# Optimization experiments

Hardware: AMD Instinct MI355X
Metric: run time of the kernel (lower is better)

The kernel has to match this reference:

```python
import jax, jax.numpy as jnp
import numpy as np

D = 256       # d_model
HEADS = 8     # n_heads
PTS = 4       # n_points
FF = 1024     # dim_feedforward
HD = D // HEADS
B, Q = 8, 900
HH, WW = 100, 100


def setup_inputs() -> dict:
    key = jax.random.key(0)
    ks = iter(jax.random.split(key, 40))
    p = lambda shape: jax.random.normal(next(ks), shape, dtype=jnp.float32) * 0.02
    inp = {
        "tgt": jax.random.normal(next(ks), (B, Q, D), dtype=jnp.float32),
        "memory": jax.random.normal(next(ks), (B, HH * WW, D), dtype=jnp.float32),
        "H": HH,
        "W": WW,
        # self-attention (nn.MultiheadAttention) params
        "in_proj_w": p((3 * D, D)), "in_proj_b": p((3 * D,)),
        "out_proj_w": p((D, D)), "out_proj_b": p((D,)),
        # layer norms
        "norm1_s": jnp.ones((D,)), "norm1_b": jnp.zeros((D,)),
        "norm2_s": jnp.ones((D,)), "norm2_b": jnp.zeros((D,)),
        "norm3_s": jnp.ones((D,)), "norm3_b": jnp.zeros((D,)),
        # deformable cross-attention params
        "vproj_w": p((D, D)), "vproj_b": p((D,)),
        "offs_w": p((HEADS * PTS * 2, D)), "offs_b": p((HEADS * PTS * 2,)),
        "attw_w": p((HEADS * PTS, D)), "attw_b": p((HEADS * PTS,)),
        "ref_w": p((2, D)), "ref_b": p((2,)),
        "cout_w": p((D, D)), "cout_b": p((D,)),
        # FFN params
        "ffn_w1": p((FF, D)), "ffn_b1": p((FF,)),
        "ffn_w2": p((D, FF)), "ffn_b2": p((D,)),
    }
    return inp


def _layer_norm(x, s, b):
    m = jnp.mean(x, -1, keepdims=True)
    v = jnp.mean((x - m) ** 2, -1, keepdims=True)
    return (x - m) * jax.lax.rsqrt(v + 1e-5) * s + b


def _mha(x, wi, bi, wo, bo):
    b, q, _ = x.shape
    qkv = x @ wi.T + bi
    qh, kh, vh = jnp.split(qkv, 3, axis=-1)
    qh = qh.reshape(b, q, HEADS, HD).transpose(0, 2, 1, 3)
    kh = kh.reshape(b, q, HEADS, HD).transpose(0, 2, 1, 3)
    vh = vh.reshape(b, q, HEADS, HD).transpose(0, 2, 1, 3)
    att = jax.nn.softmax(jnp.einsum('bhqd,bhkd->bhqk', qh, kh) / np.float32(np.sqrt(HD)), axis=-1)
    o = jnp.einsum('bhqk,bhkd->bhqd', att, vh).transpose(0, 2, 1, 3).reshape(b, q, D)
    return o @ wo.T + bo


def _deform_attn(q, mem, H, W, vproj_w, vproj_b, offs_w, offs_b, attw_w, attw_b,
                 ref_w, ref_b, cout_w, cout_b):
    b, nq, _ = q.shape
    # per-query normalized reference points (x, y) in [0,1]
    ref = jax.nn.sigmoid(q @ ref_w.T + ref_b)                         # [B,Q,2]
    offs = (q @ offs_w.T + offs_b).reshape(b, nq, HEADS, PTS, 2)      # [B,Q,h,p,2]
    attw = jax.nn.softmax((q @ attw_w.T + attw_b).reshape(b, nq, HEADS, PTS), axis=-1)
    val = (mem @ vproj_w.T + vproj_b).reshape(b, H * W, HEADS, HD).transpose(0, 2, 1, 3)  # [B,h,HW,hd]
    wh = jnp.array([W, H], dtype=q.dtype)
    loc = ref[:, :, None, None, :] + offs / wh                        # normalized sampling loc
    x = loc[..., 0] * W - 0.5                                         # pixel coords (align_corners=False)
    y = loc[..., 1] * H - 0.5
    x0 = jnp.floor(x); y0 = jnp.floor(y)
    lx = x - x0; ly = y - y0
    x0i = x0.astype(jnp.int32); y0i = y0.astype(jnp.int32)

    def gather(xi, yi):
        valid = ((xi >= 0) & (xi < W) & (yi >= 0) & (yi < H)).astype(q.dtype)
        idx = jnp.clip(yi, 0, H - 1) * W + jnp.clip(xi, 0, W - 1)     # [B,Q,h,p]
        idxt = idx.transpose(0, 2, 1, 3).reshape(b, HEADS, nq * PTS, 1)
        g = jnp.take_along_axis(val, idxt, axis=2)                    # [B,h,Q*p,hd]
        g = g.reshape(b, HEADS, nq, PTS, HD).transpose(0, 2, 1, 3, 4)  # [B,Q,h,p,hd]
        return g * valid[..., None]

    samp = (gather(x0i, y0i) * ((1 - lx) * (1 - ly))[..., None]
            + gather(x0i + 1, y0i) * (lx * (1 - ly))[..., None]
            + gather(x0i, y0i + 1) * ((1 - lx) * ly)[..., None]
            + gather(x0i + 1, y0i + 1) * (lx * ly)[..., None])        # [B,Q,h,p,hd]
    out = jnp.sum(samp * attw[..., None], axis=3).reshape(b, nq, D)
    return out @ cout_w.T + cout_b


def reference(tgt, memory, H, W, in_proj_w, in_proj_b, out_proj_w, out_proj_b,
              norm1_s, norm1_b, norm2_s, norm2_b, norm3_s, norm3_b,
              vproj_w, vproj_b, offs_w, offs_b, attw_w, attw_b, ref_w, ref_b,
              cout_w, cout_b, ffn_w1, ffn_b1, ffn_w2, ffn_b2):
    t2 = _mha(tgt, in_proj_w, in_proj_b, out_proj_w, out_proj_b)
    t = _layer_norm(tgt + t2, norm1_s, norm1_b)
    t2 = _deform_attn(t, memory, H, W, vproj_w, vproj_b, offs_w, offs_b,
                      attw_w, attw_b, ref_w, ref_b, cout_w, cout_b)
    t = _layer_norm(t + t2, norm2_s, norm2_b)
    f = jnp.maximum(t @ ffn_w1.T + ffn_b1, 0) @ ffn_w2.T + ffn_b2
    return _layer_norm(t + f, norm3_s, norm3_b)
```

## Files before the change

### kernel.cpp

```cpp
#include <hip/hip_runtime.h>
#include <hip/hip_bf16.h>

typedef __hip_bfloat16 bf16;
typedef __attribute__((ext_vector_type(8))) short short8;
typedef __attribute__((ext_vector_type(4))) float f32x4;

#define BB 8
#define QQ 900
#define DD 256
#define NH 8
#define HD 32
#define NPTS 4
#define FFD 1024
#define HH 100
#define WW2 100
#define HWTOT 10000

#define QT 64
#define KTC 128
#define NCHUNK ((QQ + KTC - 1) / KTC)
#define QB 4
#define VTP 1024

__device__ inline float tofloat(float x) { return x; }
__device__ inline float tofloat(bf16 x) { return __bfloat162float(x); }
__device__ inline float bf2f(unsigned short u) {
    return __uint_as_float(((unsigned int)u) << 16);
}
__device__ inline void storev(bf16* p, float v) { *p = __float2bfloat16(v); }
__device__ inline void storev(float* p, float v) { *p = v; }

__device__ inline void load4(const float* p, float* v) {
    const float4 t = *(const float4*)p;
    v[0] = t.x; v[1] = t.y; v[2] = t.z; v[3] = t.w;
}
__device__ inline void load4(const bf16* p, float* v) {
    const ushort4 t = *(const ushort4*)p;
    v[0] = bf2f(t.x); v[1] = bf2f(t.y); v[2] = bf2f(t.z); v[3] = bf2f(t.w);
}
__device__ inline void store4(float* p, const float* v) {
    float4 t = {v[0], v[1], v[2], v[3]};
    *(float4*)p = t;
}
__device__ inline void store4(bf16* p, const float* v) {
    bf16 t[4] = {__float2bfloat16(v[0]), __float2bfloat16(v[1]),
                 __float2bfloat16(v[2]), __float2bfloat16(v[3])};
    *(uint2*)p = *(const uint2*)t;
}

typedef __attribute__((address_space(1))) const unsigned int gas_u32;
typedef __attribute__((address_space(3))) unsigned int las_u32;
__device__ inline void gload_lds16(const bf16* g, bf16* l) {
    __builtin_amdgcn_global_load_lds(
        (gas_u32*)(unsigned long long)(const void*)g,
        (las_u32*)(unsigned int)(unsigned long long)(const void*)l, 16, 0, 0);
}

__global__ void pack_kernel(const float* __restrict__ in_proj_w, const float* __restrict__ out_proj_w,
                            const float* __restrict__ cout_w, const float* __restrict__ ffn_w1,
                            const float* __restrict__ ffn_w2, const float* __restrict__ vproj_w,
                            const float* __restrict__ offs_w, const float* __restrict__ attw_w,
                            const float* __restrict__ ref_w, const float* __restrict__ offs_b,
                            const float* __restrict__ attw_b, const float* __restrict__ ref_b,
                            const float* __restrict__ tgt, bf16* __restrict__ wpk,
                            bf16* __restrict__ tgtb, float* __restrict__ dbias,
                            bf16* __restrict__ vt) {
    const int idx = blockIdx.x * 256 + threadIdx.x;
    const int TOT = 950272 + 1843200 + 128 + 2097152;
    if (idx >= TOT) return;
    if (idx < 196608) {
        wpk[idx] = __float2bfloat16(in_proj_w[idx]);
    } else if (idx < 262144) {
        wpk[idx] = __float2bfloat16(out_proj_w[idx - 196608]);
    } else if (idx < 327680) {
        wpk[idx] = __float2bfloat16(cout_w[idx - 262144]);
    } else if (idx < 589824) {
        wpk[idx] = __float2bfloat16(ffn_w1[idx - 327680]);
    } else if (idx < 851968) {
        wpk[idx] = __float2bfloat16(ffn_w2[idx - 589824]);
    } else if (idx < 917504) {
        wpk[idx] = __float2bfloat16(vproj_w[idx - 851968]);
    } else if (idx < 950272) {
        const int j = idx - 917504;
        const int r = j >> 8, c = j & 255;
        float v = 0.f;
        if (r < 64) v = offs_w[r * 256 + c];
        else if (r < 96) v = attw_w[(r - 64) * 256 + c];
        else if (r < 98) v = ref_w[(r - 96) * 256 + c];
        wpk[idx] = __float2bfloat16(v);
    } else if (idx < 950272 + 1843200) {
        const int j = idx - 950272;
        tgtb[j] = __float2bfloat16(tgt[j]);
    } else if (idx < 950272 + 1843200 + 128) {
        const int j = idx - (950272 + 1843200);
        float v = 0.f;
        if (j < 64) v = offs_b[j];
        else if (j < 96) v = attw_b[j - 64];
        else if (j < 98) v = ref_b[j - 96];
        dbias[j] = v;
    } else {
        vt[idx - (950272 + 1843200 + 128)] = __float2bfloat16(0.f);
    }
}

template <int BM, int BN, int ACT, int VT, typename OT>
__global__ __launch_bounds__(256) void gemm_v4(const bf16* __restrict__ A,
                                               const bf16* __restrict__ W,
                                               const float* __restrict__ bias,
                                               OT* __restrict__ C, bf16* __restrict__ vt,
                                               int M, int N, int K) {
    constexpr int MACC = BM / 32;
    constexpr int NACC = BN / 32;
    constexpr int CAW = BM / 64;
    constexpr int CBW = BN / 64;
    __shared__ bf16 As[2][BM * 32];
    __shared__ bf16 Bs[2][BN * 32];
    const int bm = blockIdx.y * BM, bn = blockIdx.x * BN;
    const int tid = threadIdx.x;
    const int lane = tid & 63, wave = tid >> 6;
    const int l15 = lane & 15, g = lane >> 4;
    const int wr = wave & 1, wc = wave >> 1;
    const f32x4 zf = {0.f, 0.f, 0.f, 0.f};
    f32x4 acc[MACC][NACC];
#pragma unroll
    for (int mi = 0; mi < MACC; ++mi)
#pragma unroll
        for (int ni = 0; ni < NACC; ++ni) acc[mi][ni] = zf;

    const int s_sub = lane >> 2;
    const int s_p = lane & 3;

    const int NT = K / 32;
    int cur = 0;

    {
#pragma unroll
        for (int i = 0; i < CAW; ++i) {
            const int chunk = wave * CAW + i;
            const int r = chunk * 16 + s_sub;
            const int gp = s_p ^ ((r >> 1) & 3);
            const int grow = min(bm + r, M - 1);
            gload_lds16(A + (size_t)grow * K + 0 + gp * 8, &As[0][chunk * 512]);
        }
#pragma unroll
        for (int i = 0; i < CBW; ++i) {
            const int chunk = wave * CBW + i;
            const int r = chunk * 16 + s_sub;
            const int gp = s_p ^ ((r >> 1) & 3);
            gload_lds16(W + (size_t)(bn + r) * K + 0 + gp * 8, &Bs[0][chunk * 512]);
        }
    }
    __syncthreads();

    for (int t = 0; t < NT; ++t) {
        if (t + 1 < NT) {
            const int k0 = (t + 1) * 32;
#pragma unroll
            for (int i = 0; i < CAW; ++i) {
                const int chunk = wave * CAW + i;
                const int r = chunk * 16 + s_sub;
                const int gp = s_p ^ ((r >> 1) & 3);
                const int grow = min(bm + r, M - 1);
                gload_lds16(A + (size_t)grow * K + k0 + gp * 8, &As[cur ^ 1][chunk * 512]);
            }
#pragma unroll
            for (int i = 0; i < CBW; ++i) {
                const int chunk = wave * CBW + i;
                const int r = chunk * 16 + s_sub;
                const int gp = s_p ^ ((r >> 1) & 3);
                gload_lds16(W + (size_t)(bn + r) * K + k0 + gp * 8, &Bs[cur ^ 1][chunk * 512]);
            }
        }
        short8 af[MACC];
#pragma unroll
        for (int mi = 0; mi < MACC; ++mi) {
            const int row = wr * (BM / 2) + mi * 16 + l15;
            af[mi] = *(const short8*)&As[cur][row * 32 + (g ^ ((row >> 1) & 3)) * 8];
        }
#pragma unroll
        for (int ni = 0; ni < NACC; ++ni) {
            const int col = wc * (BN / 2) + ni * 16 + l15;
            const short8 bfv = *(const short8*)&Bs[cur][col * 32 + (g ^ ((col >> 1) & 3)) * 8];
#pragma unroll
            for (int mi = 0; mi < MACC; ++mi)
                acc[mi][ni] =
                    __builtin_amdgcn_mfma_f32_16x16x32_bf16(af[mi], bfv, acc[mi][ni], 0, 0, 0);
        }
        __syncthreads();
        cur ^= 1;
    }

#pragma unroll
    for (int ni = 0; ni < NACC; ++ni) {
        const int col = bn + wc * (BN / 2) + ni * 16 + l15;
        const float bv = bias[col];
#pragma unroll
        for (int mi = 0; mi < MACC; ++mi) {
            const int row0 = bm + wr * (BM / 2) + mi * 16 + g * 4;
            if (VT && col >= 512) {
                if (row0 < M) {
                    const int b = row0 / 900, q = row0 % 900;
                    const int hd = col - 512;
                    bf16 u4[4];
#pragma unroll
                    for (int r = 0; r < 4; ++r) u4[r] = __float2bfloat16(acc[mi][ni][r] + bv);
                    *(uint2*)&vt[((size_t)(b * NH + (hd >> 5)) * HD + (hd & 31)) * VTP + q] =
                        *(const uint2*)u4;
                }
            } else {
#pragma unroll
                for (int r = 0; r < 4; ++r) {
                    const int row = row0 + r;
                    if (row < M) {
                        float v = acc[mi][ni][r] + bv;
                        if (ACT == 1) v = fmaxf(v, 0.f);
                        if (VT)
                            storev((bf16*)C + (size_t)row * 512 + col, v);
                        else
                            storev(&C[(size_t)row * N + col], v);
                    }
                }
            }
        }
    }
}

__global__ __launch_bounds__(256) void mha_mfma_kernel(const bf16* __restrict__ qkv,
                                                       const bf16* __restrict__ vt,
                                                       bf16* __restrict__ o) {
    const int qt = blockIdx.x, h = blockIdx.y, b = blockIdx.z;
    const int tid = threadIdx.x;
    const int lane = tid & 63, wave = tid >> 6;
    const int l15 = lane & 15, g = lane >> 4;
    __shared__ bf16 KP[4096];
    __shared__ bf16 Vls[4096];
    __shared__ bf16 Pls[4][16][136];
    const size_t base = (size_t)b * QQ * 512;
    const bf16* vbase = vt + (size_t)(b * NH + h) * HD * VTP;
    const int q0 = qt * QT;

    short8 qa = {0, 0, 0, 0, 0, 0, 0, 0};
    {
        const int qg = q0 + wave * 16 + l15;
        if (qg < QQ)
            qa = *(const short8*)(qkv + base + (size_t)qg * 512 + h * HD + g * 8);
    }
    f32x4 accO[2] = {{0.f, 0.f, 0.f, 0.f}, {0.f, 0.f, 0.f, 0.f}};
    float m_run[4], l_run[4];
#pragma unroll
    for (int r = 0; r < 4; ++r) {
        m_run[r] = -1e30f;
        l_run[r] = 0.f;
    }
    const float sl2e = 0.17677669529663687f * 1.4426950408889634f;

    for (int c = 0; c < NCHUNK; ++c) {
        const int k0 = c * KTC;
        __syncthreads();
#pragma unroll
        for (int i = 0; i < 2; ++i) {
            const int r = (wave * 2 + i) * 16 + (lane >> 2);
            const int p = lane & 3;
            const int gp = p ^ ((r >> 1) & 3);
            const int kg = min(k0 + r, QQ - 1);
            gload_lds16(qkv + base + (size_t)kg * 512 + 256 + h * HD + gp * 8,
                        &KP[(wave * 2 + i) * 512]);
        }
#pragma unroll
        for (int i = 0; i < 2; ++i) {
            const int s = (wave * 2 + i) * 64 + lane;
            const int vrow = s >> 4, vp = s & 15;
            const int gp = vp ^ (vrow & 7);
            gload_lds16(vbase + (size_t)vrow * VTP + k0 + gp * 8, &Vls[(wave * 2 + i) * 512]);
        }
        __syncthreads();

        f32x4 s[8];
#pragma unroll
        for (int t = 0; t < 8; ++t) {
            const int row = t * 16 + l15;
            const short8 kb = *(const short8*)&KP[row * 32 + (g ^ ((row >> 1) & 3)) * 8];
            const f32x4 z = {0.f, 0.f, 0.f, 0.f};
            s[t] = __builtin_amdgcn_mfma_f32_16x16x32_bf16(qa, kb, z, 0, 0, 0);
        }
        float mx[4] = {-1e30f, -1e30f, -1e30f, -1e30f};
#pragma unroll
        for (int t = 0; t < 8; ++t) {
            const bool cv = (k0 + t * 16 + l15) < QQ;
#pragma unroll
            for (int r = 0; r < 4; ++r) {
                const float v = cv ? s[t][r] : -1e30f;
                s[t][r] = v;
                mx[r] = fmaxf(mx[r], v);
            }
        }
#pragma unroll
        for (int r = 0; r < 4; ++r) {
            mx[r] = fmaxf(mx[r], __shfl_xor(mx[r], 1));
            mx[r] = fmaxf(mx[r], __shfl_xor(mx[r], 2));
            mx[r] = fmaxf(mx[r], __shfl_xor(mx[r], 4));
            mx[r] = fmaxf(mx[r], __shfl_xor(mx[r], 8));
        }
        float alpha[4], rs[4];
#pragma unroll
        for (int r = 0; r < 4; ++r) {
            const float mn = fmaxf(m_run[r], mx[r]);
            alpha[r] = exp2f((m_run[r] - mn) * sl2e);
            m_run[r] = mn;
            rs[r] = 0.f;
        }
#pragma unroll
        for (int t = 0; t < 8; ++t) {
#pragma unroll
            for (int r = 0; r < 4; ++r) {
                const float p = exp2f((s[t][r] - m_run[r]) * sl2e);
                rs[r] += p;
                Pls[wave][g * 4 + r][t * 16 + l15] = __float2bfloat16(p);
            }
        }
#pragma unroll
        for (int r = 0; r < 4; ++r) {
            rs[r] += __shfl_xor(rs[r], 1);
            rs[r] += __shfl_xor(rs[r], 2);
            rs[r] += __shfl_xor(rs[r], 4);
            rs[r] += __shfl_xor(rs[r], 8);
            l_run[r] = l_run[r] * alpha[r] + rs[r];
        }
#pragma unroll
        for (int t2 = 0; t2 < 2; ++t2)
#pragma unroll
            for (int r = 0; r < 4; ++r) accO[t2][r] *= alpha[r];
#pragma unroll
        for (int s4 = 0; s4 < 4; ++s4) {
            const short8 pa = *(const short8*)&Pls[wave][l15][s4 * 32 + g * 8];
#pragma unroll
            for (int t2 = 0; t2 < 2; ++t2) {
                const int vrow = t2 * 16 + l15;
                const int pp = (s4 * 4 + g) ^ (vrow & 7);
                const short8 vb = *(const short8*)&Vls[vrow * 128 + pp * 8];
                accO[t2] = __builtin_amdgcn_mfma_f32_16x16x32_bf16(pa, vb, accO[t2], 0, 0, 0);
            }
        }
    }
#pragma unroll
    for (int r = 0; r < 4; ++r) {
        const int row = q0 + wave * 16 + g * 4 + r;
        if (row < QQ) {
            const float inv = 1.f / l_run[r];
#pragma unroll
            for (int t2 = 0; t2 < 2; ++t2) {
                storev(&o[((size_t)b * QQ + row) * DD + h * HD + t2 * 16 + l15],
                       accO[t2][r] * inv);
            }
        }
    }
}

template <typename TR, typename TO>
__global__ __launch_bounds__(256) void add_ln_kernel(const TR* __restrict__ resid,
                                                     const bf16* __restrict__ y,
                                                     const float* __restrict__ g,
                                                     const float* __restrict__ bta,
                                                     TO* __restrict__ out) {
    const int tid = threadIdx.x;
    const int lane = tid & 63, wave = tid >> 6;
    const int row = blockIdx.x * 4 + wave;
    const int c0 = lane * 4;
    const size_t base = (size_t)row * DD + c0;
    float v[4], yv[4];
    load4(resid + base, v);
    load4(y + base, yv);
#pragma unroll
    for (int j = 0; j < 4; ++j) v[j] += yv[j];
    float s = v[0] + v[1] + v[2] + v[3];
    s += __shfl_xor(s, 1);  s += __shfl_xor(s, 2);  s += __shfl_xor(s, 4);
    s += __shfl_xor(s, 8);  s += __shfl_xor(s, 16); s += __shfl_xor(s, 32);
    const float mean = s * (1.f / DD);
    float d[4];
    float q = 0.f;
#pragma unroll
    for (int j = 0; j < 4; ++j) {
        d[j] = v[j] - mean;
        q += d[j] * d[j];
    }
    q += __shfl_xor(q, 1);  q += __shfl_xor(q, 2);  q += __shfl_xor(q, 4);
    q += __shfl_xor(q, 8);  q += __shfl_xor(q, 16); q += __shfl_xor(q, 32);
    const float rstd = rsqrtf(q * (1.f / DD) + 1e-5f);
    float gv[4], bv[4], ov[4];
    load4(g + c0, gv);
    load4(bta + c0, bv);
#pragma unroll
    for (int j = 0; j < 4; ++j) ov[j] = d[j] * rstd * gv[j] + bv[j];
    store4(out + base, ov);
}

__global__ __launch_bounds__(256) void deform_gather_kernel(
    const float* __restrict__ dots, const float* __restrict__ mem,
    bf16* __restrict__ G, float* __restrict__ wsumg) {
    const int qt = blockIdx.x, b = blockIdx.y;
    const int tid = threadIdx.x;
    const int q0 = qt * QB;
    __shared__ int sidx[QB][32][4];
    __shared__ float swt[QB][32][4];

    if (tid < 128) {
        const int q = tid >> 5, hp = tid & 31;
        const float* dr = dots + ((size_t)b * QQ + q0 + q) * 128;
        const float ox = dr[hp * 2], oy = dr[hp * 2 + 1];
        float ad = dr[64 + hp];
        const float rx = dr[96], ry = dr[97];
        float mx = ad;
        mx = fmaxf(mx, __shfl_xor(mx, 1));
        mx = fmaxf(mx, __shfl_xor(mx, 2));
        float e = __expf(ad - mx);
        float sm = e;
        sm += __shfl_xor(sm, 1);
        sm += __shfl_xor(sm, 2);
        const float a = e / sm;
        const float refx = 1.f / (1.f + __expf(-rx));
        const float refy = 1.f / (1.f + __expf(-ry));
        const float x = (refx + ox * (1.f / WW2)) * WW2 - 0.5f;
        const float y = (refy + oy * (1.f / HH)) * HH - 0.5f;
        const float x0f = floorf(x), y0f = floorf(y);
        const float lx = x - x0f, ly = y - y0f;
        const int x0 = (int)x0f, y0 = (int)y0f;
        const float cw[4] = {(1 - lx) * (1 - ly), lx * (1 - ly), (1 - lx) * ly, lx * ly};
        const int cx[4] = {x0, x0 + 1, x0, x0 + 1};
        const int cy[4] = {y0, y0, y0 + 1, y0 + 1};
        float cs = 0.f;
#pragma unroll
        for (int cc = 0; cc < 4; ++cc) {
            const bool valid = cx[cc] >= 0 && cx[cc] < WW2 && cy[cc] >= 0 && cy[cc] < HH;
            const int xi = min(max(cx[cc], 0), WW2 - 1);
            const int yi = min(max(cy[cc], 0), HH - 1);
            sidx[q][hp][cc] = yi * WW2 + xi;
            const float w = valid ? a * cw[cc] : 0.f;
            swt[q][hp][cc] = w;
            cs += w;
        }
        cs += __shfl_xor(cs, 1);
        cs += __shfl_xor(cs, 2);
        if ((hp & 3) == 0) wsumg[((size_t)b * QQ + q0 + q) * NH + (hp >> 2)] = cs;
    }
    __syncthreads();

    {
        const int q = tid >> 6, cbase = (tid & 63) * 4;
        const float* mb = mem + (size_t)b * HWTOT * DD;
        bf16* gq = G + ((size_t)(b * QQ + q0 + q) * NH) * DD + cbase;
#pragma unroll
        for (int h = 0; h < NH; ++h) {
            float4 acc = {0.f, 0.f, 0.f, 0.f};
#pragma unroll
            for (int p = 0; p < NPTS; ++p) {
                const int hp = h * NPTS + p;
                const int4 ix = *(const int4*)sidx[q][hp];
                const float4 wt = *(const float4*)swt[q][hp];
                const float4 v0 = *(const float4*)(mb + (size_t)ix.x * DD + cbase);
                const float4 v1 = *(const float4*)(mb + (size_t)ix.y * DD + cbase);
                const float4 v2 = *(const float4*)(mb + (size_t)ix.z * DD + cbase);
                const float4 v3 = *(const float4*)(mb + (size_t)ix.w * DD + cbase);
                acc.x += wt.x * v0.x + wt.y * v1.x + wt.z * v2.x + wt.w * v3.x;
                acc.y += wt.x * v0.y + wt.y * v1.y + wt.z * v2.y + wt.w * v3.y;
                acc.z += wt.x * v0.z + wt.y * v1.z + wt.z * v2.z + wt.w * v3.z;
                acc.w += wt.x * v0.w + wt.y * v1.w + wt.z * v2.w + wt.w * v3.w;
            }
            bf16 out4[4] = {__float2bfloat16(acc.x), __float2bfloat16(acc.y),
                            __float2bfloat16(acc.z), __float2bfloat16(acc.w)};
            *(uint2*)(gq + (size_t)h * DD) = *(const uint2*)out4;
        }
    }
}

__global__ __launch_bounds__(256) void gemm_vproj_kernel(
    const bf16* __restrict__ G, const bf16* __restrict__ Wv,
    const float* __restrict__ vb, const float* __restrict__ wsumg,
    bf16* __restrict__ samp, int M) {
    __shared__ unsigned short As[64][40];
    __shared__ unsigned short Bs[32][40];
    const int h = blockIdx.x, bm = blockIdx.y * 64;
    const int tid = threadIdx.x;
    const int lane = tid & 63, wave = tid >> 6;
    const int l15 = lane & 15, g = lane >> 4;
    const int sr = tid >> 2, sc = (tid & 3) * 8;
    f32x4 acc[2] = {{0.f, 0.f, 0.f, 0.f}, {0.f, 0.f, 0.f, 0.f}};
    const uint4 zero4 = {0u, 0u, 0u, 0u};
    for (int k0 = 0; k0 < DD; k0 += 32) {
        __syncthreads();
        {
            const int arow = bm + sr;
            uint4 a4 = (arow < M)
                ? *(const uint4*)(G + ((size_t)arow * NH + h) * DD + k0 + sc)
                : zero4;
            *(uint4*)&As[sr][sc] = a4;
            if (sr < 32) {
                uint4 b4 = *(const uint4*)(Wv + (size_t)(h * 32 + sr) * DD + k0 + sc);
                *(uint4*)&Bs[sr][sc] = b4;
            }
        }
        __syncthreads();
        const short8 af = *(const short8*)&As[wave * 16 + l15][g * 8];
#pragma unroll
        for (int ct = 0; ct < 2; ++ct) {
            const short8 bf = *(const short8*)&Bs[ct * 16 + l15][g * 8];
            acc[ct] = __builtin_amdgcn_mfma_f32_16x16x32_bf16(af, bf, acc[ct], 0, 0, 0);
        }
    }
#pragma unroll
    for (int ct = 0; ct < 2; ++ct) {
        const int col = h * 32 + ct * 16 + l15;
        const float bv = vb[col];
#pragma unroll
        for (int r = 0; r < 4; ++r) {
            const int row = bm + wave * 16 + g * 4 + r;
            if (row < M) {
                const float v = acc[ct][r] + bv * wsumg[(size_t)row * NH + h];
                storev(&samp[(size_t)row * DD + col], v);
            }
        }
    }
}

extern "C" void kernel_launch(void* const* d_in, const int* in_sizes, int n_in,
                              void* d_out, int out_size, void* d_ws, size_t ws_size,
                              hipStream_t stream) {
    const float* tgt = (const float*)d_in[0];
    const float* memory = (const float*)d_in[1];
    const float* in_proj_w = (const float*)d_in[4];
    const float* in_proj_b = (const float*)d_in[5];
    const float* out_proj_w = (const float*)d_in[6];
    const float* out_proj_b = (const float*)d_in[7];
    const float* norm1_s = (const float*)d_in[8];
    const float* norm1_b = (const float*)d_in[9];
    const float* norm2_s = (const float*)d_in[10];
    const float* norm2_b = (const float*)d_in[11];
    const float* norm3_s = (const float*)d_in[12];
    const float* norm3_b = (const float*)d_in[13];
    const float* vproj_w = (const float*)d_in[14];
    const float* vproj_b = (const float*)d_in[15];
    const float* offs_w = (const float*)d_in[16];
    const float* offs_b = (const float*)d_in[17];
    const float* attw_w = (const float*)d_in[18];
    const float* attw_b = (const float*)d_in[19];
    const float* ref_w = (const float*)d_in[20];
    const float* ref_b = (const float*)d_in[21];
    const float* cout_w = (const float*)d_in[22];
    const float* cout_b = (const float*)d_in[23];
    const float* ffn_w1 = (const float*)d_in[24];
    const float* ffn_b1 = (const float*)d_in[25];
    const float* ffn_w2 = (const float*)d_in[26];
    const float* ffn_b2 = (const float*)d_in[27];

    const int M = BB * QQ;
    bf16* ws = (bf16*)d_ws;
    size_t off = 0;
    bf16* qkv = ws + off;  off += (size_t)M * 512;
    bf16* o = ws + off;    off += (size_t)M * DD;
    bf16* t1 = ws + off;   off += (size_t)M * DD;
    bf16* tmp = ws + off;  off += (size_t)M * DD;
    bf16* ffh = ws + off;  off += (size_t)M * FFD;
    bf16* tgtb = ws + off; off += (size_t)M * DD;
    bf16* wpk = ws + off;  off += 950272;
    float* dbias = (float*)(ws + off); off += 256;
    float* wsumg = (float*)(ws + off); off += (size_t)M * NH * 2;
    bf16* Gws = ws + off;  off += (size_t)M * NH * DD;
    bf16* vt = ws + off;   off += (size_t)BB * NH * HD * VTP;
    bf16* samp = o;
    bf16* t2n = qkv;
    float* dots = (float*)ffh;

    bf16* w_in = wpk;
    bf16* w_out = wpk + 196608;
    bf16* w_cout = wpk + 262144;
    bf16* w_ffn1 = wpk + 327680;
    bf16* w_ffn2 = wpk + 589824;
    bf16* w_vproj = wpk + 851968;
    bf16* w_dots = wpk + 917504;

    const int MT = (M + 63) / 64;
    const int LNB = M / 4;

    pack_kernel<<<(950272 + 1843200 + 128 + 2097152 + 255) / 256, 256, 0, stream>>>(
        in_proj_w, out_proj_w, cout_w, ffn_w1, ffn_w2, vproj_w, offs_w, attw_w, ref_w,
        offs_b, attw_b, ref_b, tgt, wpk, tgtb, dbias, vt);
    gemm_v4<64, 128, 0, 1, bf16><<<dim3(6, MT), 256, 0, stream>>>(tgtb, w_in, in_proj_b,
                                                                  qkv, vt, M, 768, DD);
    mha_mfma_kernel<<<dim3((QQ + QT - 1) / QT, NH, BB), 256, 0, stream>>>(qkv, vt, o);
    gemm_v4<64, 64, 0, 0, bf16><<<dim3(4, MT), 256, 0, stream>>>(o, w_out, out_proj_b,
                                                                 tmp, nullptr, M, DD, DD);
    add_ln_kernel<float, bf16><<<LNB, 256, 0, stream>>>(tgt, tmp, norm1_s, norm1_b, t1);
    gemm_v4<64, 64, 0, 0, float><<<dim3(2, MT), 256, 0, stream>>>(t1, w_dots, dbias,
                                                                  dots, nullptr, M, 128, DD);
    deform_gather_kernel<<<dim3(QQ / QB, BB), 256, 0, stream>>>(dots, memory, Gws, wsumg);
    gemm_vproj_kernel<<<dim3(NH, MT), 256, 0, stream>>>(Gws, w_vproj, vproj_b, wsumg,
                                                        samp, M);
    gemm_v4<64, 64, 0, 0, bf16><<<dim3(4, MT), 256, 0, stream>>>(samp, w_cout, cout_b,
                                                                 tmp, nullptr, M, DD, DD);
    add_ln_kernel<bf16, bf16><<<LNB, 256, 0, stream>>>(t1, tmp, norm2_s, norm2_b, t2n);
    gemm_v4<64, 128, 1, 0, bf16><<<dim3(8, MT), 256, 0, stream>>>(t2n, w_ffn1, ffn_b1,
                                                                  ffh, nullptr, M, FFD, DD);
    gemm_v4<64, 64, 0, 0, bf16><<<dim3(4, MT), 256, 0, stream>>>(ffh, w_ffn2, ffn_b2,
                                                                 tmp, nullptr, M, DD, FFD);
    add_ln_kernel<bf16, float><<<LNB, 256, 0, stream>>>(t2n, tmp, norm3_s, norm3_b,
                                                        (float*)d_out);
}
```

Measured before the change: 337.7 us.

## Replace double-buffered GEMM with full-K-chunk 64x64 tiled GEMM kernel

The templated double-buffered GEMM that stepped K by 32 is replaced with a fixed 64x64 tile kernel. It loads a whole 256-wide K chunk of A and W into LDS at once, using an XOR swizzle on 16-byte slots, then runs eight MFMA steps per chunk. This cuts the number of barriers and load rounds per tile, and the grids for the QKV and FFN1 GEMMs double to give more blocks. In exchange, global loads no longer overlap with compute inside the chunk, and each block now uses 64 KB of LDS, which may reduce occupancy.

```diff
diff --git a/kernel.cpp b/kernel.cpp
--- a/kernel.cpp
+++ b/kernel.cpp
@@ -103,100 +103,67 @@
     }
 }
 
-template <int BM, int BN, int ACT, int VT, typename OT>
-__global__ __launch_bounds__(256) void gemm_v4(const bf16* __restrict__ A,
+template <int ACT, int VT, typename OT>
+__global__ __launch_bounds__(256) void gemm_v5(const bf16* __restrict__ A,
                                                const bf16* __restrict__ W,
                                                const float* __restrict__ bias,
                                                OT* __restrict__ C, bf16* __restrict__ vt,
                                                int M, int N, int K) {
-    constexpr int MACC = BM / 32;
-    constexpr int NACC = BN / 32;
-    constexpr int CAW = BM / 64;
-    constexpr int CBW = BN / 64;
-    __shared__ bf16 As[2][BM * 32];
-    __shared__ bf16 Bs[2][BN * 32];
-    const int bm = blockIdx.y * BM, bn = blockIdx.x * BN;
+    __shared__ bf16 As[64 * 256];
+    __shared__ bf16 Bs[64 * 256];
+    const int bm = blockIdx.y * 64, bn = blockIdx.x * 64;
     const int tid = threadIdx.x;
     const int lane = tid & 63, wave = tid >> 6;
     const int l15 = lane & 15, g = lane >> 4;
     const int wr = wave & 1, wc = wave >> 1;
     const f32x4 zf = {0.f, 0.f, 0.f, 0.f};
-    f32x4 acc[MACC][NACC];
-#pragma unroll
-    for (int mi = 0; mi < MACC; ++mi)
-#pragma unroll
-        for (int ni = 0; ni < NACC; ++ni) acc[mi][ni] = zf;
-
-    const int s_sub = lane >> 2;
-    const int s_p = lane & 3;
-
-    const int NT = K / 32;
-    int cur = 0;
-
-    {
-#pragma unroll
-        for (int i = 0; i < CAW; ++i) {
-            const int chunk = wave * CAW + i;
-            const int r = chunk * 16 + s_sub;
-            const int gp = s_p ^ ((r >> 1) & 3);
-            const int grow = min(bm + r, M - 1);
-            gload_lds16(A + (size_t)grow * K + 0 + gp * 8, &As[0][chunk * 512]);
-        }
-#pragma unroll
-        for (int i = 0; i < CBW; ++i) {
-            const int chunk = wave * CBW + i;
-            const int r = chunk * 16 + s_sub;
-            const int gp = s_p ^ ((r >> 1) & 3);
-            gload_lds16(W + (size_t)(bn + r) * K + 0 + gp * 8, &Bs[0][chunk * 512]);
-        }
-    }
-    __syncthreads();
-
-    for (int t = 0; t < NT; ++t) {
-        if (t + 1 < NT) {
-            const int k0 = (t + 1) * 32;
-#pragma unroll
-            for (int i = 0; i < CAW; ++i) {
-                const int chunk = wave * CAW + i;
-                const int r = chunk * 16 + s_sub;
-                const int gp = s_p ^ ((r >> 1) & 3);
-                const int grow = min(bm + r, M - 1);
-                gload_lds16(A + (size_t)grow * K + k0 + gp * 8, &As[cur ^ 1][chunk * 512]);
-            }
-#pragma unroll
-            for (int i = 0; i < CBW; ++i) {
-                const int chunk = wave * CBW + i;
-                const int r = chunk * 16 + s_sub;
-                const int gp = s_p ^ ((r >> 1) & 3);
-                gload_lds16(W + (size_t)(bn + r) * K + k0 + gp * 8, &Bs[cur ^ 1][chunk * 512]);
-            }
-        }
-        short8 af[MACC];
-#pragma unroll
-        for (int mi = 0; mi < MACC; ++mi) {
-            const int row = wr * (BM / 2) + mi * 16 + l15;
-            af[mi] = *(const short8*)&As[cur][row * 32 + (g ^ ((row >> 1) & 3)) * 8];
-        }
-#pragma unroll
-        for (int ni = 0; ni < NACC; ++ni) {
-            const int col = wc * (BN / 2) + ni * 16 + l15;
-            const short8 bfv = *(const short8*)&Bs[cur][col * 32 + (g ^ ((col >> 1) & 3)) * 8];
-#pragma unroll
-            for (int mi = 0; mi < MACC; ++mi)
-                acc[mi][ni] =
-                    __builtin_amdgcn_mfma_f32_16x16x32_bf16(af[mi], bfv, acc[mi][ni], 0, 0, 0);
-        }
+    f32x4 acc[2][2] = {{zf, zf}, {zf, zf}};
+
+    for (int kc = 0; kc < K; kc += 256) {
         __syncthreads();
-        cur ^= 1;
-    }
-
-#pragma unroll
-    for (int ni = 0; ni < NACC; ++ni) {
-        const int col = bn + wc * (BN / 2) + ni * 16 + l15;
+#pragma unroll
+        for (int j = 0; j < 8; ++j) {
+            const int bslot = wave * 64 + j * 256;
+            const int slot = bslot + lane;
+            const int row = slot >> 5;
+            const int off = ((slot & 31) << 4) ^ ((row & 7) << 4);
+            const int grow = min(bm + row, M - 1);
+            gload_lds16(A + (size_t)grow * K + kc + (off >> 1), &As[bslot * 8]);
+            gload_lds16(W + (size_t)(bn + row) * K + kc + (off >> 1), &Bs[bslot * 8]);
+        }
+        __syncthreads();
+
+#pragma unroll
+        for (int kk = 0; kk < 8; ++kk) {
+            short8 af[2], bfv[2];
+#pragma unroll
+            for (int mi = 0; mi < 2; ++mi) {
+                const int row = wr * 32 + mi * 16 + l15;
+                const int byte = (row * 512 + kk * 64 + g * 16) ^ ((row & 7) << 4);
+                af[mi] = *(const short8*)((const char*)As + byte);
+            }
+#pragma unroll
+            for (int ni = 0; ni < 2; ++ni) {
+                const int col = wc * 32 + ni * 16 + l15;
+                const int byte = (col * 512 + kk * 64 + g * 16) ^ ((col & 7) << 4);
+                bfv[ni] = *(const short8*)((const char*)Bs + byte);
+            }
+#pragma unroll
+            for (int ni = 0; ni < 2; ++ni)
+#pragma unroll
+                for (int mi = 0; mi < 2; ++mi)
+                    acc[mi][ni] = __builtin_amdgcn_mfma_f32_16x16x32_bf16(af[mi], bfv[ni],
+                                                                          acc[mi][ni], 0, 0, 0);
+        }
+    }
+
+#pragma unroll
+    for (int ni = 0; ni < 2; ++ni) {
+        const int col = bn + wc * 32 + ni * 16 + l15;
         const float bv = bias[col];
 #pragma unroll
-        for (int mi = 0; mi < MACC; ++mi) {
-            const int row0 = bm + wr * (BM / 2) + mi * 16 + g * 4;
+        for (int mi = 0; mi < 2; ++mi) {
+            const int row0 = bm + wr * 32 + mi * 16 + g * 4;
             if (VT && col >= 512) {
                 if (row0 < M) {
                     const int b = row0 / 900, q = row0 % 900;
@@ -583,24 +550,24 @@
     pack_kernel<<<(950272 + 1843200 + 128 + 2097152 + 255) / 256, 256, 0, stream>>>(
         in_proj_w, out_proj_w, cout_w, ffn_w1, ffn_w2, vproj_w, offs_w, attw_w, ref_w,
         offs_b, attw_b, ref_b, tgt, wpk, tgtb, dbias, vt);
-    gemm_v4<64, 128, 0, 1, bf16><<<dim3(6, MT), 256, 0, stream>>>(tgtb, w_in, in_proj_b,
-                                                                  qkv, vt, M, 768, DD);
+    gemm_v5<0, 1, bf16><<<dim3(12, MT), 256, 0, stream>>>(tgtb, w_in, in_proj_b,
+                                                          qkv, vt, M, 768, DD);
     mha_mfma_kernel<<<dim3((QQ + QT - 1) / QT, NH, BB), 256, 0, stream>>>(qkv, vt, o);
-    gemm_v4<64, 64, 0, 0, bf16><<<dim3(4, MT), 256, 0, stream>>>(o, w_out, out_proj_b,
-                                                                 tmp, nullptr, M, DD, DD);
+    gemm_v5<0, 0, bf16><<<dim3(4, MT), 256, 0, stream>>>(o, w_out, out_proj_b,
+                                                         tmp, nullptr, M, DD, DD);
     add_ln_kernel<float, bf16><<<LNB, 256, 0, stream>>>(tgt, tmp, norm1_s, norm1_b, t1);
-    gemm_v4<64, 64, 0, 0, float><<<dim3(2, MT), 256, 0, stream>>>(t1, w_dots, dbias,
-                                                                  dots, nullptr, M, 128, DD);
+    gemm_v5<0, 0, float><<<dim3(2, MT), 256, 0, stream>>>(t1, w_dots, dbias,
+                                                          dots, nullptr, M, 128, DD);
     deform_gather_kernel<<<dim3(QQ / QB, BB), 256, 0, stream>>>(dots, memory, Gws, wsumg);
     gemm_vproj_kernel<<<dim3(NH, MT), 256, 0, stream>>>(Gws, w_vproj, vproj_b, wsumg,
                                                         samp, M);
-    gemm_v4<64, 64, 0, 0, bf16><<<dim3(4, MT), 256, 0, stream>>>(samp, w_cout, cout_b,
-                                                                 tmp, nullptr, M, DD, DD);
+    gemm_v5<0, 0, bf16><<<dim3(4, MT), 256, 0, stream>>>(samp, w_cout, cout_b,
+                                                         tmp, nullptr, M, DD, DD);
     add_ln_kernel<bf16, bf16><<<LNB, 256, 0, stream>>>(t1, tmp, norm2_s, norm2_b, t2n);
-    gemm_v4<64, 128, 1, 0, bf16><<<dim3(8, MT), 256, 0, stream>>>(t2n, w_ffn1, ffn_b1,
-                                                                  ffh, nullptr, M, FFD, DD);
-    gemm_v4<64, 64, 0, 0, bf16><<<dim3(4, MT), 256, 0, stream>>>(ffh, w_ffn2, ffn_b2,
-                                                                 tmp, nullptr, M, DD, FFD);
+    gemm_v5<1, 0, bf16><<<dim3(16, MT), 256, 0, stream>>>(t2n, w_ffn1, ffn_b1,
+                                                          ffh, nullptr, M, FFD, DD);
+    gemm_v5<0, 0, bf16><<<dim3(4, MT), 256, 0, stream>>>(ffh, w_ffn2, ffn_b2,
+                                                         tmp, nullptr, M, DD, FFD);
     add_ln_kernel<bf16, float><<<LNB, 256, 0, stream>>>(t2n, tmp, norm3_s, norm3_b,
                                                         (float*)d_out);
 }
```

Result: no change. 343.7 us (+1.8%).
